# Kernel tuning notes

Hardware: AMD Instinct MI355X
Metric: run time of the kernel (lower is better)

## Reference

```python
import jax, jax.numpy as jnp
import numpy as np

B, N, NP, NS = 8, 4096, 1024, 32
CF = 64            # input point-feature channels; in_channel = 3 + CF = 67
MLP = [64, 128, 256]
EPS = 1e-5         # BatchNorm eps (torch default)


def setup_inputs() -> dict:
    key = jax.random.key(0)
    ks = jax.random.split(key, 8)
    inp = {
        "xyz": jax.random.normal(ks[0], (B, N, 3), jnp.float32),
        "points": jax.random.normal(ks[1], (B, CF, N), jnp.float32),
        "sample_idx": jax.random.randint(ks[2], (B, NP), 0, N, dtype=jnp.int32),
        "neighbor_idx": jax.random.randint(ks[3], (B, NP, NS), 0, N, dtype=jnp.int32),
    }
    c = 3 + CF
    for i, o in enumerate(MLP):
        wk = jax.random.fold_in(ks[4], i)
        inp[f"W{i}"] = jax.random.normal(wk, (o, c), jnp.float32) * (1.0 / np.sqrt(c))
        inp[f"b{i}"] = jnp.zeros((o,), jnp.float32)
        inp[f"gamma{i}"] = jnp.ones((o,), jnp.float32)
        inp[f"beta{i}"] = jnp.zeros((o,), jnp.float32)
        c = o
    return inp


def _forward(xyz, points, sample_idx, neighbor_idx, params):
    # xyz: (B,N,3)  points: (B,CF,N)
    new_xyz = jnp.take_along_axis(xyz, sample_idx[:, :, None], axis=1)        # (B,NP,3)
    nbr_xyz = jax.vmap(lambda x, idx: x[idx])(xyz, neighbor_idx)               # (B,NP,NS,3)
    rel = nbr_xyz - new_xyz[:, :, None, :]                                     # (B,NP,NS,3)
    nbr_feat = jax.vmap(lambda f, idx: f[:, idx])(points, neighbor_idx)        # (B,CF,NP,NS)
    x = jnp.concatenate([rel.transpose(0, 3, 1, 2), nbr_feat], axis=1)         # (B,3+CF,NP,NS)
    # 1x1 Conv2d -> BatchNorm2d (training-mode batch stats) -> ReLU stack
    for W, b, g, be in params:
        x = jnp.einsum('oc,bcps->bops', W, x) + b[None, :, None, None]
        mu = x.mean(axis=(0, 2, 3), keepdims=True)
        var = x.var(axis=(0, 2, 3), keepdims=True)
        x = g[None, :, None, None] * (x - mu) * jax.lax.rsqrt(var + EPS) + be[None, :, None, None]
        x = jax.nn.relu(x)
    new_points = x.max(axis=-1)                                                # (B,C_out,NP)
    return new_xyz, new_points


def reference(xyz, points, sample_idx, neighbor_idx,
              W0, b0, gamma0, beta0,
              W1, b1, gamma1, beta1,
              W2, b2, gamma2, beta2):
    params = [(W0, b0, gamma0, beta0), (W1, b1, gamma1, beta1), (W2, b2, gamma2, beta2)]
    return _forward(xyz, points, sample_idx, neighbor_idx, params)
```

## Files before the change

kernel.cpp:

```cpp
#include <hip/hip_runtime.h>

typedef unsigned short u16;
typedef unsigned int u32;
typedef __attribute__((ext_vector_type(8))) short short8;
typedef __attribute__((ext_vector_type(16))) float f32x16;

#define BB 8
#define NN 4096
#define NPP 1024
#define NSS 32
#define CFF 64
#define C0 67
#define H0 64
#define H1 128
#define H2 256
#define MTOT (BB*NPP*NSS)
#define BN_EPS 1e-5f
#define INV_M (1.0f/262144.0f)

#define MFMA32(a,b,c) __builtin_amdgcn_mfma_f32_32x32x16_bf16(a,b,c,0,0,0)

__device__ __forceinline__ float bf2f(u16 h){ return __uint_as_float(((u32)h)<<16); }
__device__ __forceinline__ u16 f2bf(float f){
  u32 u = __float_as_uint(f);
  u32 r = (u + 0x7fffu + ((u>>16)&1u)) >> 16;
  return (u16)r;
}
__device__ __forceinline__ u32 pack2(float a, float b){
  return (u32)f2bf(a) | ((u32)f2bf(b)<<16);
}

#define WS_NEED 46280704u

__global__ __launch_bounds__(256) void k_setup(
    const float* __restrict__ xyz, const float* __restrict__ points,
    const int* __restrict__ sidx,
    const float* __restrict__ W0, const float* __restrict__ W1, const float* __restrict__ W2,
    u16* __restrict__ ptsT, u16* __restrict__ Wt0c, u16* __restrict__ Wt1c,
    u16* __restrict__ Wt2c, float* __restrict__ out_newxyz)
{
  int blk = blockIdx.x, tid = threadIdx.x;
  if (blk < 512) {
    __shared__ float t[64][68];
    int b = blk >> 6, n0 = (blk & 63) << 6;
    for (int it = 0; it < 4; ++it) {
      int u = it*256 + tid;
      int nq = u & 15, c = u >> 4;
      float4 v = *(const float4*)&points[(size_t)(b*CFF + c)*NN + n0 + nq*4];
      *(float4*)&t[c][nq*4] = v;
    }
    __syncthreads();
    for (int it = 0; it < 2; ++it) {
      int u = it*256 + tid;
      int oct = u & 7, n = u >> 3;
      u16 pk[8];
#pragma unroll
      for (int j = 0; j < 8; ++j) pk[j] = f2bf(t[oct*8 + j][n]);
      *(uint4*)&ptsT[((size_t)(b*NN + n0 + n))*CFF + oct*8] = *(uint4*)pk;
    }
  } else if (blk < 544) {
    int t0 = (blk - 512)*256 + tid;
    int b = t0 >> 10;
    int s = sidx[t0];
    for (int k = 0; k < 3; ++k)
      out_newxyz[(size_t)t0*3 + k] = xyz[((size_t)(b*NN + s))*3 + k];
  } else if (blk == 544) {
    for (int i = 0; i < 24; ++i) {
      int e = i*256 + tid;
      int kc = e >> 9, o = (e >> 3) & 63, j = e & 7, k = kc*8 + j;
      float v = (k < 64) ? W0[o*C0 + 3 + k] : ((k < 67) ? W0[o*C0 + (k - 64)] : 0.f);
      Wt0c[e] = f2bf(v);
    }
  } else if (blk == 545) {
    for (int i = 0; i < 32; ++i) {
      int e = i*256 + tid;
      int kc = e >> 10, n = (e >> 3) & 127, j = e & 7;
      Wt1c[e] = f2bf(W1[n*H0 + kc*8 + j]);
    }
  } else {
    int base = (blk - 546) * 4096;
    for (int i = 0; i < 16; ++i) {
      int e = base + i*256 + tid;
      int kc = e >> 11, n = (e >> 3) & 255, j = e & 7;
      Wt2c[e] = f2bf(W2[n*H1 + kc*8 + j]);
    }
  }
}

__global__ __launch_bounds__(256) void k_xyz_only(
    const float* __restrict__ xyz, const int* __restrict__ sidx, float* __restrict__ out_newxyz)
{
  int t0 = blockIdx.x*256 + threadIdx.x;
  int b = t0 >> 10;
  int s = sidx[t0];
  for (int k = 0; k < 3; ++k)
    out_newxyz[(size_t)t0*3 + k] = xyz[((size_t)(b*NN + s))*3 + k];
}

__global__ __launch_bounds__(256) void k_l0(
    const float* __restrict__ xyz, const int* __restrict__ sidx, const int* __restrict__ nidx,
    const u16* __restrict__ ptsT, const u16* __restrict__ Wt0c,
    u16* __restrict__ y0, float* __restrict__ stats)
{
  __shared__ u16 XLc[12*128*8];
  __shared__ u16 W0c[12*64*8];
  int tid = threadIdx.x;
  int m0 = blockIdx.x * 128;
  int b = m0 >> 15;

  for (int i = 0; i < 3; ++i)
    ((uint4*)W0c)[i*256 + tid] = ((const uint4*)Wt0c)[i*256 + tid];

  int pos = tid & 127, half = tid >> 7;
  int m = m0 + pos;
  int nb = nidx[m];
  {
    const uint4* prow = (const uint4*)(ptsT + ((size_t)(b*NN + nb))*CFF + half*32);
    uint4 h0 = prow[0], h1 = prow[1], h2 = prow[2], h3 = prow[3];
    *(uint4*)&XLc[((half*4+0)*128 + pos)*8] = h0;
    *(uint4*)&XLc[((half*4+1)*128 + pos)*8] = h1;
    *(uint4*)&XLc[((half*4+2)*128 + pos)*8] = h2;
    *(uint4*)&XLc[((half*4+3)*128 + pos)*8] = h3;
    if (half == 0) {
      int p = (m & 32767) >> 5;
      int sp = sidx[b*NPP + p];
      float r0 = xyz[((size_t)(b*NN+nb))*3+0] - xyz[((size_t)(b*NN+sp))*3+0];
      float r1 = xyz[((size_t)(b*NN+nb))*3+1] - xyz[((size_t)(b*NN+sp))*3+1];
      float r2 = xyz[((size_t)(b*NN+nb))*3+2] - xyz[((size_t)(b*NN+sp))*3+2];
      uint4 v = { pack2(r0, r1), pack2(r2, 0.f), 0u, 0u };
      *(uint4*)&XLc[(8*128 + pos)*8] = v;
    } else {
      uint4 z = {0u,0u,0u,0u};
      *(uint4*)&XLc[(9*128 + pos)*8]  = z;
      *(uint4*)&XLc[(10*128 + pos)*8] = z;
      *(uint4*)&XLc[(11*128 + pos)*8] = z;
    }
  }
  __syncthreads();

  int lane = tid & 63, wv = tid >> 6;
  int l31 = lane & 31, kh = lane >> 5;
  int nt = wv & 1, mtb = (wv >> 1) * 2;
  f32x16 acc[2];
  for (int mi = 0; mi < 2; ++mi) for (int r = 0; r < 16; ++r) acc[mi][r] = 0.f;

  for (int kt = 0; kt < 6; ++kt) {
    int ck = kt*2 + kh;
    short8 bfrag = *(const short8*)&W0c[(ck*64 + nt*32 + l31)*8];
    for (int mi = 0; mi < 2; ++mi) {
      short8 afrag = *(const short8*)&XLc[(ck*128 + (mtb+mi)*32 + l31)*8];
      acc[mi] = MFMA32(afrag, bfrag, acc[mi]);
    }
  }

  float s = 0.f, q = 0.f;
  for (int mi = 0; mi < 2; ++mi)
    for (int r = 0; r < 16; ++r) { float y = acc[mi][r]; s += y; q += y*y; }
  s += __shfl_xor(s, 32); q += __shfl_xor(q, 32);
  if (lane < 32) {
    int slot = blockIdx.x & 7;
    atomicAdd(&stats[slot*256 + nt*32 + lane], s);
    atomicAdd(&stats[2048 + slot*256 + nt*32 + lane], q);
  }

  __syncthreads();
  {
    int chx = (nt*32 + l31) ^ (kh*32);
#pragma unroll
    for (int mi = 0; mi < 2; ++mi)
#pragma unroll
      for (int r = 0; r < 16; ++r) {
        int mm = (mtb+mi)*32 + (r&3) + 8*(r>>2) + 4*kh;
        XLc[mm*64 + chx] = f2bf(acc[mi][r]);
      }
  }
  __syncthreads();
  {
    uint4* dst = (uint4*)(y0 + (size_t)m0*H0);
#pragma unroll
    for (int i = 0; i < 4; ++i) {
      int t16 = i*256 + tid;
      int mrow = t16 >> 3, ch0 = (t16 & 7)*8;
      int idx = mrow*64 + (ch0 ^ (32*((mrow>>2)&1)));
      dst[t16] = *(const uint4*)&XLc[idx];
    }
  }
}

__global__ __launch_bounds__(256, 4) void k_l1s(
    const u16* __restrict__ y0, const u16* __restrict__ Wt1c,
    const float* __restrict__ g0, const float* __restrict__ e0,
    const float* __restrict__ stIn, float* __restrict__ stOut)
{
  __shared__ u16 X0c[8*128*8];
  __shared__ float scl0[64], sft0[64];
  int tid = threadIdx.x;
  int m0 = blockIdx.x * 128;
  int lane = tid & 63, wv = tid >> 6;
  int l31 = lane & 31, kh = lane >> 5;

  int pos = tid & 127, half = tid >> 7;
  u16 hs[32];
  {
    const u16* row = y0 + (size_t)(m0 + pos)*H0 + half*32;
#pragma unroll
    for (int t = 0; t < 4; ++t) *(uint4*)&hs[t*8] = ((const uint4*)row)[t];
  }
  short8 b1[4];
#pragma unroll
  for (int kt = 0; kt < 4; ++kt)
    b1[kt] = *(const short8*)&Wt1c[((kt*2 + kh)*128 + wv*32 + l31)*8];

  if (tid < 64) {
    float s = 0.f, q = 0.f;
    for (int sl = 0; sl < 8; ++sl) { s += stIn[sl*256 + tid]; q += stIn[2048 + sl*256 + tid]; }
    float mu = s*INV_M, var = q*INV_M - mu*mu;
    float sc = g0[tid] * rsqrtf(var + BN_EPS);
    scl0[tid] = sc; sft0[tid] = e0[tid] - mu*sc;
  }
  __syncthreads();

  {
    u16 ob[32];
#pragma unroll
    for (int j = 0; j < 32; ++j) {
      int c = half*32 + j;
      ob[j] = f2bf(fmaxf(fmaf(scl0[c], bf2f(hs[j]), sft0[c]), 0.f));
    }
#pragma unroll
    for (int t = 0; t < 4; ++t)
      *(uint4*)&X0c[((half*4+t)*128 + pos)*8] = *(uint4*)&ob[t*8];
  }
  __syncthreads();

  f32x16 acc[4];
#pragma unroll
  for (int mt = 0; mt < 4; ++mt) for (int r = 0; r < 16; ++r) acc[mt][r] = 0.f;

#pragma unroll
  for (int kt = 0; kt < 4; ++kt) {
    int ck = kt*2 + kh;
#pragma unroll
    for (int mt = 0; mt < 4; ++mt) {
      short8 afrag = *(const short8*)&X0c[(ck*128 + mt*32 + l31)*8];
      acc[mt] = MFMA32(afrag, b1[kt], acc[mt]);
    }
  }

  float s = 0.f, q = 0.f;
#pragma unroll
  for (int mt = 0; mt < 4; ++mt)
#pragma unroll
    for (int r = 0; r < 16; ++r) { float y = acc[mt][r]; s += y; q += y*y; }
  s += __shfl_xor(s, 32); q += __shfl_xor(q, 32);
  if (lane < 32) {
    int slot = blockIdx.x & 7;
    atomicAdd(&stOut[slot*256 + wv*32 + lane], s);
    atomicAdd(&stOut[2048 + slot*256 + wv*32 + lane], q);
  }
}

__global__ __launch_bounds__(256, 4) void k_l2f(
    const u16* __restrict__ y0, const u16* __restrict__ Wt1c, const u16* __restrict__ Wt2c,
    const float* __restrict__ g0, const float* __restrict__ e0,
    const float* __restrict__ g1, const float* __restrict__ e1,
    const float* __restrict__ st0, const float* __restrict__ st1, float* __restrict__ stOut,
    u16* __restrict__ mxp, u16* __restrict__ mnp)
{
  __shared__ u16 X0c[8*64*8];
  __shared__ u16 X1c[16*64*8];
  __shared__ float scl0[64], sft0[64], scl1[128], sft1[128];
  int tid = threadIdx.x;
  int m0 = blockIdx.x * 64;
  int lane = tid & 63, wv = tid >> 6;
  int l31 = lane & 31, kh = lane >> 5;

  int pos = tid & 63, grp = tid >> 6;
  u16 hs[16];
  {
    const u16* row = y0 + (size_t)(m0 + pos)*H0 + grp*16;
    *(uint4*)&hs[0] = ((const uint4*)row)[0];
    *(uint4*)&hs[8] = ((const uint4*)row)[1];
  }
  short8 b1[4];
#pragma unroll
  for (int kt = 0; kt < 4; ++kt)
    b1[kt] = *(const short8*)&Wt1c[((kt*2 + kh)*128 + wv*32 + l31)*8];

  if (tid < 64) {
    float s = 0.f, q = 0.f;
    for (int sl = 0; sl < 8; ++sl) { s += st0[sl*256 + tid]; q += st0[2048 + sl*256 + tid]; }
    float mu = s*INV_M, var = q*INV_M - mu*mu;
    float sc = g0[tid] * rsqrtf(var + BN_EPS);
    scl0[tid] = sc; sft0[tid] = e0[tid] - mu*sc;
  }
  if (tid < 128) {
    float s = 0.f, q = 0.f;
    for (int sl = 0; sl < 8; ++sl) { s += st1[sl*256 + tid]; q += st1[2048 + sl*256 + tid]; }
    float mu = s*INV_M, var = q*INV_M - mu*mu;
    float sc = g1[tid] * rsqrtf(var + BN_EPS);
    scl1[tid] = sc; sft1[tid] = e1[tid] - mu*sc;
  }
  __syncthreads();

  {
    u16 ob[16];
#pragma unroll
    for (int j = 0; j < 16; ++j) {
      int c = grp*16 + j;
      ob[j] = f2bf(fmaxf(fmaf(scl0[c], bf2f(hs[j]), sft0[c]), 0.f));
    }
    *(uint4*)&X0c[((2*grp)*64 + pos)*8]   = *(uint4*)&ob[0];
    *(uint4*)&X0c[((2*grp+1)*64 + pos)*8] = *(uint4*)&ob[8];
  }
  __syncthreads();

  f32x16 acc1[2];
#pragma unroll
  for (int mt = 0; mt < 2; ++mt) for (int r = 0; r < 16; ++r) acc1[mt][r] = 0.f;
#pragma unroll
  for (int kt = 0; kt < 4; ++kt) {
    int ck = kt*2 + kh;
#pragma unroll
    for (int mt = 0; mt < 2; ++mt) {
      short8 afrag = *(const short8*)&X0c[(ck*64 + mt*32 + l31)*8];
      acc1[mt] = MFMA32(afrag, b1[kt], acc1[mt]);
    }
  }

  {
    int ch1 = wv*32 + l31;
    int cb = ch1 >> 3, cr = ch1 & 7, sw = cb & 3;
    float sc1 = scl1[ch1], sf1 = sft1[ch1];
#pragma unroll
    for (int mt = 0; mt < 2; ++mt)
#pragma unroll
      for (int r = 0; r < 16; ++r) {
        int mm = mt*32 + (r&3) + 8*(r>>2) + 4*kh;
        X1c[(cb*64 + (mm ^ sw))*8 + cr] = f2bf(fmaxf(fmaf(sc1, acc1[mt][r], sf1), 0.f));
      }
  }
  __syncthreads();

  f32x16 acc2[2][2];
#pragma unroll
  for (int nt = 0; nt < 2; ++nt) for (int mt = 0; mt < 2; ++mt)
    for (int r = 0; r < 16; ++r) acc2[nt][mt][r] = 0.f;

#pragma unroll
  for (int k4 = 0; k4 < 8; ++k4) {
    int ck = k4*2 + kh;
    int sw = ck & 3;
    short8 bf_[2];
#pragma unroll
    for (int nt = 0; nt < 2; ++nt)
      bf_[nt] = *(const short8*)&Wt2c[(ck*256 + wv*64 + nt*32 + l31)*8];
    short8 a[2];
#pragma unroll
    for (int mt = 0; mt < 2; ++mt)
      a[mt] = *(const short8*)&X1c[(ck*64 + ((mt*32 + l31) ^ sw))*8];
#pragma unroll
    for (int nt = 0; nt < 2; ++nt)
#pragma unroll
      for (int mt = 0; mt < 2; ++mt)
        acc2[nt][mt] = MFMA32(a[mt], bf_[nt], acc2[nt][mt]);
  }

  int slot = blockIdx.x & 7;
#pragma unroll
  for (int nt = 0; nt < 2; ++nt) {
    float s = 0.f, q = 0.f;
    float mx[2] = {-3.0e38f, -3.0e38f}, mn[2] = {3.0e38f, 3.0e38f};
#pragma unroll
    for (int mt = 0; mt < 2; ++mt)
#pragma unroll
      for (int r = 0; r < 16; ++r) {
        float y = acc2[nt][mt][r];
        s += y; q += y*y;
        mx[mt] = fmaxf(mx[mt], y); mn[mt] = fminf(mn[mt], y);
      }
    s += __shfl_xor(s, 32); q += __shfl_xor(q, 32);
    mx[0] = fmaxf(mx[0], __shfl_xor(mx[0], 32));
    mx[1] = fmaxf(mx[1], __shfl_xor(mx[1], 32));
    mn[0] = fminf(mn[0], __shfl_xor(mn[0], 32));
    mn[1] = fminf(mn[1], __shfl_xor(mn[1], 32));
    if (lane < 32) {
      int c = wv*64 + nt*32 + lane;
      atomicAdd(&stOut[slot*256 + c], s);
      atomicAdd(&stOut[2048 + slot*256 + c], q);
#pragma unroll
      for (int mt = 0; mt < 2; ++mt) {
        size_t pr = (size_t)blockIdx.x*2 + mt;
        mxp[pr*H2 + c] = f2bf(mx[mt]);
        mnp[pr*H2 + c] = f2bf(mn[mt]);
      }
    }
  }
}

__global__ __launch_bounds__(256) void k_final(
    const u16* __restrict__ mxp, const u16* __restrict__ mnp,
    const float* __restrict__ gma, const float* __restrict__ bta,
    const float* __restrict__ stIn, float* __restrict__ out_np)
{
  __shared__ float tmp[256][33];
  int tid = threadIdx.x;
  int b = blockIdx.x >> 5;
  int p0 = (blockIdx.x & 31) * 32;

  float s = 0.f, q = 0.f;
  for (int sl = 0; sl < 8; ++sl) { s += stIn[sl*256 + tid]; q += stIn[2048 + sl*256 + tid]; }
  float mu = s*INV_M, var = q*INV_M - mu*mu;
  float sc = gma[tid] * rsqrtf(var + BN_EPS);
  float sh = bta[tid] - mu*sc;

  for (int pp = 0; pp < 32; ++pp) {
    size_t base = ((size_t)(b*NPP + p0 + pp))*H2 + tid;
    float xv = bf2f(mxp[base]), nv = bf2f(mnp[base]);
    float v = (sc >= 0.f) ? fmaf(sc, xv, sh) : fmaf(sc, nv, sh);
    tmp[tid][pp] = fmaxf(v, 0.f);
  }
  __syncthreads();

  int pl = tid & 31, cg = tid >> 5;
  for (int cc = 0; cc < 32; ++cc) {
    int c = cc*8 + cg;
    out_np[((size_t)b*H2 + c)*NPP + p0 + pl] = tmp[c][pl];
  }
}

extern "C" void kernel_launch(void* const* d_in, const int* in_sizes, int n_in,
                              void* d_out, int out_size, void* d_ws, size_t ws_size,
                              hipStream_t stream)
{
  const float* xyz    = (const float*)d_in[0];
  const float* points = (const float*)d_in[1];
  const int*   sidx   = (const int*)d_in[2];
  const int*   nidx   = (const int*)d_in[3];
  const float* W0 = (const float*)d_in[4];
  const float* g0 = (const float*)d_in[6];
  const float* e0 = (const float*)d_in[7];
  const float* W1 = (const float*)d_in[8];
  const float* g1 = (const float*)d_in[10];
  const float* e1 = (const float*)d_in[11];
  const float* W2 = (const float*)d_in[12];
  const float* g2 = (const float*)d_in[14];
  const float* e2 = (const float*)d_in[15];

  float* out_xyz = (float*)d_out;
  float* out_np  = out_xyz + (size_t)BB*NPP*3;

  if (ws_size < (size_t)WS_NEED) {
    hipMemsetAsync(out_np, 0, (size_t)BB*H2*NPP*4, stream);
    k_xyz_only<<<32, 256, 0, stream>>>(xyz, sidx, out_xyz);
    return;
  }

  char* ws = (char*)d_ws;
  float* stats = (float*)(ws + 0);
  u16*   Wt0c  = (u16*)(ws + 49152);
  u16*   Wt1c  = (u16*)(ws + 61440);
  u16*   Wt2c  = (u16*)(ws + 77824);
  u16*   ptsT  = (u16*)(ws + 143360);
  u16*   y0    = (u16*)(ws + 4337664);
  u16*   mxp   = (u16*)(ws + 37892096);
  u16*   mnp   = (u16*)(ws + 42086400);

  hipMemsetAsync(stats, 0, 3*4096*sizeof(float), stream);
  k_setup<<<554, 256, 0, stream>>>(xyz, points, sidx, W0, W1, W2,
                                   ptsT, Wt0c, Wt1c, Wt2c, out_xyz);
  k_l0<<<MTOT/128, 256, 0, stream>>>(xyz, sidx, nidx, ptsT, Wt0c, y0, stats);
  k_l1s<<<MTOT/128, 256, 0, stream>>>(y0, Wt1c, g0, e0, stats, stats + 4096);
  k_l2f<<<MTOT/64, 256, 0, stream>>>(y0, Wt1c, Wt2c, g0, e0, g1, e1,
                                     stats, stats + 4096, stats + 8192, mxp, mnp);
  k_final<<<256, 256, 0, stream>>>(mxp, mnp, g2, e2, stats + 8192, out_np);
}
```

Before: 170.5 us.

## Process multiple row tiles per block in layer kernels with prefetch

The three layer kernels now have each block loop over several 128- or 64-row tiles: two in k_l0 and k_l1s, four in k_l2f. Grids shrink to 1024 blocks. This spreads the weight staging, BN scale computation and statistics atomics over more rows, and software-prefetches the next tile's y0 rows into registers while the current tile computes. The cost is more registers, the risk of lower occupancy, and fewer blocks to hide latency.

```diff
diff --git a/kernel.cpp b/kernel.cpp
--- a/kernel.cpp
+++ b/kernel.cpp
@@ -97,7 +97,7 @@
     out_newxyz[(size_t)t0*3 + k] = xyz[((size_t)(b*NN + s))*3 + k];
 }
 
-__global__ __launch_bounds__(256) void k_l0(
+__global__ __launch_bounds__(256, 4) void k_l0(
     const float* __restrict__ xyz, const int* __restrict__ sidx, const int* __restrict__ nidx,
     const u16* __restrict__ ptsT, const u16* __restrict__ Wt0c,
     u16* __restrict__ y0, float* __restrict__ stats)
@@ -105,85 +105,97 @@
   __shared__ u16 XLc[12*128*8];
   __shared__ u16 W0c[12*64*8];
   int tid = threadIdx.x;
-  int m0 = blockIdx.x * 128;
-  int b = m0 >> 15;
 
   for (int i = 0; i < 3; ++i)
     ((uint4*)W0c)[i*256 + tid] = ((const uint4*)Wt0c)[i*256 + tid];
 
   int pos = tid & 127, half = tid >> 7;
-  int m = m0 + pos;
-  int nb = nidx[m];
-  {
-    const uint4* prow = (const uint4*)(ptsT + ((size_t)(b*NN + nb))*CFF + half*32);
-    uint4 h0 = prow[0], h1 = prow[1], h2 = prow[2], h3 = prow[3];
-    *(uint4*)&XLc[((half*4+0)*128 + pos)*8] = h0;
-    *(uint4*)&XLc[((half*4+1)*128 + pos)*8] = h1;
-    *(uint4*)&XLc[((half*4+2)*128 + pos)*8] = h2;
-    *(uint4*)&XLc[((half*4+3)*128 + pos)*8] = h3;
-    if (half == 0) {
-      int p = (m & 32767) >> 5;
-      int sp = sidx[b*NPP + p];
-      float r0 = xyz[((size_t)(b*NN+nb))*3+0] - xyz[((size_t)(b*NN+sp))*3+0];
-      float r1 = xyz[((size_t)(b*NN+nb))*3+1] - xyz[((size_t)(b*NN+sp))*3+1];
-      float r2 = xyz[((size_t)(b*NN+nb))*3+2] - xyz[((size_t)(b*NN+sp))*3+2];
-      uint4 v = { pack2(r0, r1), pack2(r2, 0.f), 0u, 0u };
-      *(uint4*)&XLc[(8*128 + pos)*8] = v;
-    } else {
-      uint4 z = {0u,0u,0u,0u};
-      *(uint4*)&XLc[(9*128 + pos)*8]  = z;
-      *(uint4*)&XLc[(10*128 + pos)*8] = z;
-      *(uint4*)&XLc[(11*128 + pos)*8] = z;
-    }
-  }
-  __syncthreads();
-
   int lane = tid & 63, wv = tid >> 6;
   int l31 = lane & 31, kh = lane >> 5;
   int nt = wv & 1, mtb = (wv >> 1) * 2;
-  f32x16 acc[2];
-  for (int mi = 0; mi < 2; ++mi) for (int r = 0; r < 16; ++r) acc[mi][r] = 0.f;
-
-  for (int kt = 0; kt < 6; ++kt) {
-    int ck = kt*2 + kh;
-    short8 bfrag = *(const short8*)&W0c[(ck*64 + nt*32 + l31)*8];
-    for (int mi = 0; mi < 2; ++mi) {
-      short8 afrag = *(const short8*)&XLc[(ck*128 + (mtb+mi)*32 + l31)*8];
-      acc[mi] = MFMA32(afrag, bfrag, acc[mi]);
-    }
-  }
-
-  float s = 0.f, q = 0.f;
-  for (int mi = 0; mi < 2; ++mi)
-    for (int r = 0; r < 16; ++r) { float y = acc[mi][r]; s += y; q += y*y; }
-  s += __shfl_xor(s, 32); q += __shfl_xor(q, 32);
+
+  float sA = 0.f, qA = 0.f;
+
+  for (int it = 0; it < 2; ++it) {
+    int m0 = (blockIdx.x*2 + it) * 128;
+    int b = m0 >> 15;
+    int m = m0 + pos;
+    int nb = nidx[m];
+
+    if (it) __syncthreads();
+    {
+      const uint4* prow = (const uint4*)(ptsT + ((size_t)(b*NN + nb))*CFF + half*32);
+      uint4 h0 = prow[0], h1 = prow[1], h2 = prow[2], h3 = prow[3];
+      *(uint4*)&XLc[((half*4+0)*128 + pos)*8] = h0;
+      *(uint4*)&XLc[((half*4+1)*128 + pos)*8] = h1;
+      *(uint4*)&XLc[((half*4+2)*128 + pos)*8] = h2;
+      *(uint4*)&XLc[((half*4+3)*128 + pos)*8] = h3;
+      if (half == 0) {
+        int p = (m & 32767) >> 5;
+        int sp = sidx[b*NPP + p];
+        float r0 = xyz[((size_t)(b*NN+nb))*3+0] - xyz[((size_t)(b*NN+sp))*3+0];
+        float r1 = xyz[((size_t)(b*NN+nb))*3+1] - xyz[((size_t)(b*NN+sp))*3+1];
+        float r2 = xyz[((size_t)(b*NN+nb))*3+2] - xyz[((size_t)(b*NN+sp))*3+2];
+        uint4 v = { pack2(r0, r1), pack2(r2, 0.f), 0u, 0u };
+        *(uint4*)&XLc[(8*128 + pos)*8] = v;
+      } else {
+        uint4 z = {0u,0u,0u,0u};
+        *(uint4*)&XLc[(9*128 + pos)*8]  = z;
+        *(uint4*)&XLc[(10*128 + pos)*8] = z;
+        *(uint4*)&XLc[(11*128 + pos)*8] = z;
+      }
+    }
+    __syncthreads();
+
+    f32x16 acc[2];
+#pragma unroll
+    for (int mi = 0; mi < 2; ++mi) for (int r = 0; r < 16; ++r) acc[mi][r] = 0.f;
+
+#pragma unroll
+    for (int kt = 0; kt < 6; ++kt) {
+      int ck = kt*2 + kh;
+      short8 bfrag = *(const short8*)&W0c[(ck*64 + nt*32 + l31)*8];
+#pragma unroll
+      for (int mi = 0; mi < 2; ++mi) {
+        short8 afrag = *(const short8*)&XLc[(ck*128 + (mtb+mi)*32 + l31)*8];
+        acc[mi] = MFMA32(afrag, bfrag, acc[mi]);
+      }
+    }
+
+#pragma unroll
+    for (int mi = 0; mi < 2; ++mi)
+#pragma unroll
+      for (int r = 0; r < 16; ++r) { float y = acc[mi][r]; sA += y; qA += y*y; }
+
+    __syncthreads();
+    {
+      int chx = (nt*32 + l31) ^ (kh*32);
+#pragma unroll
+      for (int mi = 0; mi < 2; ++mi)
+#pragma unroll
+        for (int r = 0; r < 16; ++r) {
+          int mm = (mtb+mi)*32 + (r&3) + 8*(r>>2) + 4*kh;
+          XLc[mm*64 + chx] = f2bf(acc[mi][r]);
+        }
+    }
+    __syncthreads();
+    {
+      uint4* dst = (uint4*)(y0 + (size_t)m0*H0);
+#pragma unroll
+      for (int i = 0; i < 4; ++i) {
+        int t16 = i*256 + tid;
+        int mrow = t16 >> 3, ch0 = (t16 & 7)*8;
+        int idx = mrow*64 + (ch0 ^ (32*((mrow>>2)&1)));
+        dst[t16] = *(const uint4*)&XLc[idx];
+      }
+    }
+  }
+
+  sA += __shfl_xor(sA, 32); qA += __shfl_xor(qA, 32);
   if (lane < 32) {
     int slot = blockIdx.x & 7;
-    atomicAdd(&stats[slot*256 + nt*32 + lane], s);
-    atomicAdd(&stats[2048 + slot*256 + nt*32 + lane], q);
-  }
-
-  __syncthreads();
-  {
-    int chx = (nt*32 + l31) ^ (kh*32);
-#pragma unroll
-    for (int mi = 0; mi < 2; ++mi)
-#pragma unroll
-      for (int r = 0; r < 16; ++r) {
-        int mm = (mtb+mi)*32 + (r&3) + 8*(r>>2) + 4*kh;
-        XLc[mm*64 + chx] = f2bf(acc[mi][r]);
-      }
-  }
-  __syncthreads();
-  {
-    uint4* dst = (uint4*)(y0 + (size_t)m0*H0);
-#pragma unroll
-    for (int i = 0; i < 4; ++i) {
-      int t16 = i*256 + tid;
-      int mrow = t16 >> 3, ch0 = (t16 & 7)*8;
-      int idx = mrow*64 + (ch0 ^ (32*((mrow>>2)&1)));
-      dst[t16] = *(const uint4*)&XLc[idx];
-    }
+    atomicAdd(&stats[slot*256 + nt*32 + lane], sA);
+    atomicAdd(&stats[2048 + slot*256 + nt*32 + lane], qA);
   }
 }
 
@@ -195,14 +207,13 @@
   __shared__ u16 X0c[8*128*8];
   __shared__ float scl0[64], sft0[64];
   int tid = threadIdx.x;
-  int m0 = blockIdx.x * 128;
   int lane = tid & 63, wv = tid >> 6;
   int l31 = lane & 31, kh = lane >> 5;
-
   int pos = tid & 127, half = tid >> 7;
-  u16 hs[32];
+
+  u16 hs[32], hn[32];
   {
-    const u16* row = y0 + (size_t)(m0 + pos)*H0 + half*32;
+    const u16* row = y0 + ((size_t)blockIdx.x*256 + pos)*H0 + half*32;
 #pragma unroll
     for (int t = 0; t < 4; ++t) *(uint4*)&hs[t*8] = ((const uint4*)row)[t];
   }
@@ -218,45 +229,57 @@
     float sc = g0[tid] * rsqrtf(var + BN_EPS);
     scl0[tid] = sc; sft0[tid] = e0[tid] - mu*sc;
   }
-  __syncthreads();
-
-  {
-    u16 ob[32];
-#pragma unroll
-    for (int j = 0; j < 32; ++j) {
-      int c = half*32 + j;
-      ob[j] = f2bf(fmaxf(fmaf(scl0[c], bf2f(hs[j]), sft0[c]), 0.f));
-    }
-#pragma unroll
-    for (int t = 0; t < 4; ++t)
-      *(uint4*)&X0c[((half*4+t)*128 + pos)*8] = *(uint4*)&ob[t*8];
-  }
-  __syncthreads();
-
-  f32x16 acc[4];
-#pragma unroll
-  for (int mt = 0; mt < 4; ++mt) for (int r = 0; r < 16; ++r) acc[mt][r] = 0.f;
-
-#pragma unroll
-  for (int kt = 0; kt < 4; ++kt) {
-    int ck = kt*2 + kh;
-#pragma unroll
-    for (int mt = 0; mt < 4; ++mt) {
-      short8 afrag = *(const short8*)&X0c[(ck*128 + mt*32 + l31)*8];
-      acc[mt] = MFMA32(afrag, b1[kt], acc[mt]);
-    }
-  }
-
-  float s = 0.f, q = 0.f;
-#pragma unroll
-  for (int mt = 0; mt < 4; ++mt)
-#pragma unroll
-    for (int r = 0; r < 16; ++r) { float y = acc[mt][r]; s += y; q += y*y; }
-  s += __shfl_xor(s, 32); q += __shfl_xor(q, 32);
+
+  float sA = 0.f, qA = 0.f;
+
+  for (int it = 0; it < 2; ++it) {
+    __syncthreads();
+    {
+      u16 ob[32];
+#pragma unroll
+      for (int j = 0; j < 32; ++j) {
+        int c = half*32 + j;
+        ob[j] = f2bf(fmaxf(fmaf(scl0[c], bf2f(hs[j]), sft0[c]), 0.f));
+      }
+#pragma unroll
+      for (int t = 0; t < 4; ++t)
+        *(uint4*)&X0c[((half*4+t)*128 + pos)*8] = *(uint4*)&ob[t*8];
+    }
+    if (it == 0) {
+      const u16* row = y0 + ((size_t)blockIdx.x*256 + 128 + pos)*H0 + half*32;
+#pragma unroll
+      for (int t = 0; t < 4; ++t) *(uint4*)&hn[t*8] = ((const uint4*)row)[t];
+    }
+    __syncthreads();
+
+    f32x16 acc[4];
+#pragma unroll
+    for (int mt = 0; mt < 4; ++mt) for (int r = 0; r < 16; ++r) acc[mt][r] = 0.f;
+#pragma unroll
+    for (int kt = 0; kt < 4; ++kt) {
+      int ck = kt*2 + kh;
+#pragma unroll
+      for (int mt = 0; mt < 4; ++mt) {
+        short8 afrag = *(const short8*)&X0c[(ck*128 + mt*32 + l31)*8];
+        acc[mt] = MFMA32(afrag, b1[kt], acc[mt]);
+      }
+    }
+#pragma unroll
+    for (int mt = 0; mt < 4; ++mt)
+#pragma unroll
+      for (int r = 0; r < 16; ++r) { float y = acc[mt][r]; sA += y; qA += y*y; }
+
+    if (it == 0) {
+#pragma unroll
+      for (int j = 0; j < 32; ++j) hs[j] = hn[j];
+    }
+  }
+
+  sA += __shfl_xor(sA, 32); qA += __shfl_xor(qA, 32);
   if (lane < 32) {
     int slot = blockIdx.x & 7;
-    atomicAdd(&stOut[slot*256 + wv*32 + lane], s);
-    atomicAdd(&stOut[2048 + slot*256 + wv*32 + lane], q);
+    atomicAdd(&stOut[slot*256 + wv*32 + lane], sA);
+    atomicAdd(&stOut[2048 + slot*256 + wv*32 + lane], qA);
   }
 }
 
@@ -271,14 +294,14 @@
   __shared__ u16 X1c[16*64*8];
   __shared__ float scl0[64], sft0[64], scl1[128], sft1[128];
   int tid = threadIdx.x;
-  int m0 = blockIdx.x * 64;
   int lane = tid & 63, wv = tid >> 6;
   int l31 = lane & 31, kh = lane >> 5;
-
   int pos = tid & 63, grp = tid >> 6;
-  u16 hs[16];
+  int slot = blockIdx.x & 7;
+
+  u16 hs[16], hn[16];
   {
-    const u16* row = y0 + (size_t)(m0 + pos)*H0 + grp*16;
+    const u16* row = y0 + ((size_t)blockIdx.x*256 + pos)*H0 + grp*16;
     *(uint4*)&hs[0] = ((const uint4*)row)[0];
     *(uint4*)&hs[8] = ((const uint4*)row)[1];
   }
@@ -301,99 +324,122 @@
     float sc = g1[tid] * rsqrtf(var + BN_EPS);
     scl1[tid] = sc; sft1[tid] = e1[tid] - mu*sc;
   }
-  __syncthreads();
-
-  {
-    u16 ob[16];
-#pragma unroll
-    for (int j = 0; j < 16; ++j) {
-      int c = grp*16 + j;
-      ob[j] = f2bf(fmaxf(fmaf(scl0[c], bf2f(hs[j]), sft0[c]), 0.f));
-    }
-    *(uint4*)&X0c[((2*grp)*64 + pos)*8]   = *(uint4*)&ob[0];
-    *(uint4*)&X0c[((2*grp+1)*64 + pos)*8] = *(uint4*)&ob[8];
-  }
-  __syncthreads();
-
-  f32x16 acc1[2];
-#pragma unroll
-  for (int mt = 0; mt < 2; ++mt) for (int r = 0; r < 16; ++r) acc1[mt][r] = 0.f;
-#pragma unroll
-  for (int kt = 0; kt < 4; ++kt) {
-    int ck = kt*2 + kh;
-#pragma unroll
-    for (int mt = 0; mt < 2; ++mt) {
-      short8 afrag = *(const short8*)&X0c[(ck*64 + mt*32 + l31)*8];
-      acc1[mt] = MFMA32(afrag, b1[kt], acc1[mt]);
-    }
-  }
-
-  {
-    int ch1 = wv*32 + l31;
-    int cb = ch1 >> 3, cr = ch1 & 7, sw = cb & 3;
-    float sc1 = scl1[ch1], sf1 = sft1[ch1];
-#pragma unroll
-    for (int mt = 0; mt < 2; ++mt)
-#pragma unroll
-      for (int r = 0; r < 16; ++r) {
-        int mm = mt*32 + (r&3) + 8*(r>>2) + 4*kh;
-        X1c[(cb*64 + (mm ^ sw))*8 + cr] = f2bf(fmaxf(fmaf(sc1, acc1[mt][r], sf1), 0.f));
-      }
-  }
-  __syncthreads();
-
-  f32x16 acc2[2][2];
-#pragma unroll
-  for (int nt = 0; nt < 2; ++nt) for (int mt = 0; mt < 2; ++mt)
-    for (int r = 0; r < 16; ++r) acc2[nt][mt][r] = 0.f;
-
-#pragma unroll
-  for (int k4 = 0; k4 < 8; ++k4) {
-    int ck = k4*2 + kh;
-    int sw = ck & 3;
-    short8 bf_[2];
-#pragma unroll
-    for (int nt = 0; nt < 2; ++nt)
-      bf_[nt] = *(const short8*)&Wt2c[(ck*256 + wv*64 + nt*32 + l31)*8];
-    short8 a[2];
-#pragma unroll
-    for (int mt = 0; mt < 2; ++mt)
-      a[mt] = *(const short8*)&X1c[(ck*64 + ((mt*32 + l31) ^ sw))*8];
-#pragma unroll
-    for (int nt = 0; nt < 2; ++nt)
+
+  float sac[2] = {0.f, 0.f}, qac[2] = {0.f, 0.f};
+
+  for (int it = 0; it < 4; ++it) {
+    int mt0 = blockIdx.x*4 + it;
+
+    __syncthreads();
+
+    {
+      u16 ob[16];
+#pragma unroll
+      for (int j = 0; j < 16; ++j) {
+        int c = grp*16 + j;
+        ob[j] = f2bf(fmaxf(fmaf(scl0[c], bf2f(hs[j]), sft0[c]), 0.f));
+      }
+      *(uint4*)&X0c[((2*grp)*64 + pos)*8]   = *(uint4*)&ob[0];
+      *(uint4*)&X0c[((2*grp+1)*64 + pos)*8] = *(uint4*)&ob[8];
+    }
+    __syncthreads();
+
+    f32x16 acc1[2];
+#pragma unroll
+    for (int mt = 0; mt < 2; ++mt) for (int r = 0; r < 16; ++r) acc1[mt][r] = 0.f;
+#pragma unroll
+    for (int kt = 0; kt < 4; ++kt) {
+      int ck = kt*2 + kh;
+#pragma unroll
+      for (int mt = 0; mt < 2; ++mt) {
+        short8 afrag = *(const short8*)&X0c[(ck*64 + mt*32 + l31)*8];
+        acc1[mt] = MFMA32(afrag, b1[kt], acc1[mt]);
+      }
+    }
+
+    {
+      int ch1 = wv*32 + l31;
+      int cb = ch1 >> 3, cr = ch1 & 7, sw = cb & 3;
+      float sc1 = scl1[ch1], sf1 = sft1[ch1];
 #pragma unroll
       for (int mt = 0; mt < 2; ++mt)
-        acc2[nt][mt] = MFMA32(a[mt], bf_[nt], acc2[nt][mt]);
-  }
-
-  int slot = blockIdx.x & 7;
+#pragma unroll
+        for (int r = 0; r < 16; ++r) {
+          int mm = mt*32 + (r&3) + 8*(r>>2) + 4*kh;
+          X1c[(cb*64 + (mm ^ sw))*8 + cr] = f2bf(fmaxf(fmaf(sc1, acc1[mt][r], sf1), 0.f));
+        }
+    }
+    if (it < 3) {
+      const u16* row = y0 + ((size_t)(mt0+1)*64 + pos)*H0 + grp*16;
+      *(uint4*)&hn[0] = ((const uint4*)row)[0];
+      *(uint4*)&hn[8] = ((const uint4*)row)[1];
+    }
+    __syncthreads();
+
+    f32x16 acc2[2][2];
+#pragma unroll
+    for (int nt = 0; nt < 2; ++nt) for (int mt = 0; mt < 2; ++mt)
+      for (int r = 0; r < 16; ++r) acc2[nt][mt][r] = 0.f;
+
+#pragma unroll
+    for (int k4 = 0; k4 < 8; ++k4) {
+      int ck = k4*2 + kh;
+      int sw = ck & 3;
+      short8 bf_[2];
+#pragma unroll
+      for (int nt = 0; nt < 2; ++nt)
+        bf_[nt] = *(const short8*)&Wt2c[(ck*256 + wv*64 + nt*32 + l31)*8];
+      short8 a[2];
+#pragma unroll
+      for (int mt = 0; mt < 2; ++mt)
+        a[mt] = *(const short8*)&X1c[(ck*64 + ((mt*32 + l31) ^ sw))*8];
+#pragma unroll
+      for (int nt = 0; nt < 2; ++nt)
+#pragma unroll
+        for (int mt = 0; mt < 2; ++mt)
+          acc2[nt][mt] = MFMA32(a[mt], bf_[nt], acc2[nt][mt]);
+    }
+
+#pragma unroll
+    for (int nt = 0; nt < 2; ++nt) {
+      float mx[2] = {-3.0e38f, -3.0e38f}, mn[2] = {3.0e38f, 3.0e38f};
+#pragma unroll
+      for (int mt = 0; mt < 2; ++mt)
+#pragma unroll
+        for (int r = 0; r < 16; ++r) {
+          float y = acc2[nt][mt][r];
+          sac[nt] += y; qac[nt] += y*y;
+          mx[mt] = fmaxf(mx[mt], y); mn[mt] = fminf(mn[mt], y);
+        }
+      mx[0] = fmaxf(mx[0], __shfl_xor(mx[0], 32));
+      mx[1] = fmaxf(mx[1], __shfl_xor(mx[1], 32));
+      mn[0] = fminf(mn[0], __shfl_xor(mn[0], 32));
+      mn[1] = fminf(mn[1], __shfl_xor(mn[1], 32));
+      if (lane < 32) {
+        int c = wv*64 + nt*32 + lane;
+#pragma unroll
+        for (int mt = 0; mt < 2; ++mt) {
+          size_t pr = (size_t)mt0*2 + mt;
+          mxp[pr*H2 + c] = f2bf(mx[mt]);
+          mnp[pr*H2 + c] = f2bf(mn[mt]);
+        }
+      }
+    }
+
+    if (it < 3) {
+#pragma unroll
+      for (int j = 0; j < 16; ++j) hs[j] = hn[j];
+    }
+  }
+
 #pragma unroll
   for (int nt = 0; nt < 2; ++nt) {
-    float s = 0.f, q = 0.f;
-    float mx[2] = {-3.0e38f, -3.0e38f}, mn[2] = {3.0e38f, 3.0e38f};
-#pragma unroll
-    for (int mt = 0; mt < 2; ++mt)
-#pragma unroll
-      for (int r = 0; r < 16; ++r) {
-        float y = acc2[nt][mt][r];
-        s += y; q += y*y;
-        mx[mt] = fmaxf(mx[mt], y); mn[mt] = fminf(mn[mt], y);
-      }
+    float s = sac[nt], q = qac[nt];
     s += __shfl_xor(s, 32); q += __shfl_xor(q, 32);
-    mx[0] = fmaxf(mx[0], __shfl_xor(mx[0], 32));
-    mx[1] = fmaxf(mx[1], __shfl_xor(mx[1], 32));
-    mn[0] = fminf(mn[0], __shfl_xor(mn[0], 32));
-    mn[1] = fminf(mn[1], __shfl_xor(mn[1], 32));
     if (lane < 32) {
       int c = wv*64 + nt*32 + lane;
       atomicAdd(&stOut[slot*256 + c], s);
       atomicAdd(&stOut[2048 + slot*256 + c], q);
-#pragma unroll
-      for (int mt = 0; mt < 2; ++mt) {
-        size_t pr = (size_t)blockIdx.x*2 + mt;
-        mxp[pr*H2 + c] = f2bf(mx[mt]);
-        mnp[pr*H2 + c] = f2bf(mn[mt]);
-      }
     }
   }
 }
@@ -469,9 +515,9 @@
   hipMemsetAsync(stats, 0, 3*4096*sizeof(float), stream);
   k_setup<<<554, 256, 0, stream>>>(xyz, points, sidx, W0, W1, W2,
                                    ptsT, Wt0c, Wt1c, Wt2c, out_xyz);
-  k_l0<<<MTOT/128, 256, 0, stream>>>(xyz, sidx, nidx, ptsT, Wt0c, y0, stats);
-  k_l1s<<<MTOT/128, 256, 0, stream>>>(y0, Wt1c, g0, e0, stats, stats + 4096);
-  k_l2f<<<MTOT/64, 256, 0, stream>>>(y0, Wt1c, Wt2c, g0, e0, g1, e1,
-                                     stats, stats + 4096, stats + 8192, mxp, mnp);
+  k_l0<<<1024, 256, 0, stream>>>(xyz, sidx, nidx, ptsT, Wt0c, y0, stats);
+  k_l1s<<<1024, 256, 0, stream>>>(y0, Wt1c, g0, e0, stats, stats + 4096);
+  k_l2f<<<1024, 256, 0, stream>>>(y0, Wt1c, Wt2c, g0, e0, g1, e1,
+                                  stats, stats + 4096, stats + 8192, mxp, mnp);
   k_final<<<256, 256, 0, stream>>>(mxp, mnp, g2, e2, stats + 8192, out_np);
 }
```

New measurement: 222.4 us. +30.4%, slower.
